# Kernel optimization log

Hardware: AMD Instinct MI355X
Metric: run time of the kernel (lower is better)

## Reference

```python
import jax, jax.numpy as jnp
import numpy as np

INPUT_DIM, HIDDEN_DIM, OUTPUT_DIM = 64, 256, 32
BATCH, SEQ = 256, 1024
# AutoNCP(256, 32, sparsity_level=0.5): motor=32, command=max(int(0.4*224),1)=89, inter=135
LAYER_HID = [135, 89, 32]
LAYER_IN = [INPUT_DIM, 135, 89]


def setup_inputs() -> dict:
    key = jax.random.key(0)
    ks = iter(jax.random.split(key, 64))
    d = {}
    d["x"] = jax.random.normal(next(ks), (BATCH, SEQ, INPUT_DIM), dtype=jnp.float32)
    for l, (fin, hid) in enumerate(zip(LAYER_IN, LAYER_HID)):
        sp = jax.random.bernoulli(next(ks), 0.5, (hid, fin))
        d[f"mask{l}"] = jnp.concatenate([sp, jnp.ones((hid, hid), dtype=bool)], axis=1)
        scale = 1.0 / np.sqrt(fin + hid)
        for name in ("W1", "W2", "Wa", "Wb"):
            d[f"{name}_{l}"] = jax.random.normal(next(ks), (hid, fin + hid), dtype=jnp.float32) * scale
        for name in ("b1", "b2", "ba", "bb"):
            d[f"{name}_{l}"] = jnp.zeros((hid,), dtype=jnp.float32)
    d["fc_W"] = jax.random.normal(next(ks), (HIDDEN_DIM, HIDDEN_DIM), dtype=jnp.float32) * (1.0 / np.sqrt(HIDDEN_DIM))
    d["fc_b"] = jnp.zeros((HIDDEN_DIM,), dtype=jnp.float32)
    return d


def _cfc_cell(inp, h, mask, W1, b1, W2, b2, Wa, ba, Wb, bb):
    # ncps CfCCell, mode='default', no backbone, ts = 1.0
    x = jnp.concatenate([inp, h], axis=1)
    m = mask.astype(W1.dtype)
    ff1 = jnp.tanh(x @ (W1 * m).T + b1)
    ff2 = jnp.tanh(x @ (W2 * m).T + b2)
    t = jax.nn.sigmoid(x @ Wa.T + ba + x @ Wb.T + bb)  # sigmoid(t_a*ts + t_b), ts=1
    return ff1 * (1.0 - t) + t * ff2


def _forward(x, masks, layer_params, fc_W, fc_b):
    B = x.shape[0]
    init = tuple(jnp.zeros((B, h), dtype=x.dtype) for h in LAYER_HID)

    def step(carry, xt):
        hs = list(carry)
        inp = xt
        for l in range(3):  # inter -> command -> motor (WiredCfCCell)
            hs[l] = _cfc_cell(inp, hs[l], masks[l], *layer_params[l])
            inp = hs[l]
        return tuple(hs), None

    carry, _ = jax.lax.scan(step, init, jnp.swapaxes(x, 0, 1))  # scan over time [T,B,D]
    hn = jnp.concatenate(carry, axis=1)  # [B, HIDDEN_DIM] full state
    return hn @ fc_W.T + fc_b


def reference(x, mask0, mask1, mask2,
              W1_0, b1_0, W2_0, b2_0, Wa_0, ba_0, Wb_0, bb_0,
              W1_1, b1_1, W2_1, b2_1, Wa_1, ba_1, Wb_1, bb_1,
              W1_2, b1_2, W2_2, b2_2, Wa_2, ba_2, Wb_2, bb_2,
              fc_W, fc_b):
    masks = (mask0, mask1, mask2)
    lp = ((W1_0, b1_0, W2_0, b2_0, Wa_0, ba_0, Wb_0, bb_0),
          (W1_1, b1_1, W2_1, b2_1, Wa_1, ba_1, Wb_1, bb_1),
          (W1_2, b1_2, W2_2, b2_2, Wa_2, ba_2, Wb_2, bb_2))
    return _forward(x, masks, lp, fc_W, fc_b)
```

## Files before the change

kernel.cpp:

```cpp
#include <hip/hip_runtime.h>


typedef _Float16 half2v __attribute__((ext_vector_type(2)));
typedef _Float16 half8v __attribute__((ext_vector_type(8)));
typedef int      int4v  __attribute__((ext_vector_type(4)));

#define NBLK   256
#define NTHR   512
#define TSTEPS 1024
#define KPAD   224
#define KHALF  112

struct Ptrs {
    const float* x;
    const unsigned int* msk[3];
    const float* W1[3];
    const float* W2[3];
    const float* Wa[3];
    const float* Wb[3];
    const float* b1[3];
    const float* b2[3];
    const float* ba[3];
    const float* bb[3];
    const float* fcW;
    const float* fcb;
};

__device__ __forceinline__ float fexp2(float x) {
#if __has_builtin(__builtin_amdgcn_exp2f)
    return __builtin_amdgcn_exp2f(x);
#else
    return exp2f(x);
#endif
}
__device__ __forceinline__ float frcp(float x) {
#if __has_builtin(__builtin_amdgcn_rcpf)
    return __builtin_amdgcn_rcpf(x);
#else
    return 1.0f / x;
#endif
}
__device__ __forceinline__ float fsig(float x) {
    return frcp(1.0f + fexp2(-1.442695041f * x));
}
__device__ __forceinline__ float ftanh(float x) {
    return 2.0f * frcp(1.0f + fexp2(-2.885390082f * x)) - 1.0f;
}

#if __has_builtin(__builtin_amdgcn_fdot2)
#define FD(a, b, c) __builtin_amdgcn_fdot2((a), (b), (c), false)
#else
__device__ __forceinline__ float fd_fallback(half2v a, half2v b, float c) {
    return c + (float)a[0] * (float)b[0] + (float)a[1] * (float)b[1];
}
#define FD(a, b, c) fd_fallback((a), (b), (c))
#endif

__device__ __forceinline__ half2v h2(_Float16 a, _Float16 b) { return half2v{a, b}; }

__device__ __forceinline__ half8v dpp_xor2(half8v v) {
    int4v a = __builtin_bit_cast(int4v, v);
    int4v r;
    r[0] = __builtin_amdgcn_update_dpp(0, a[0], 0x4E, 0xF, 0xF, true);
    r[1] = __builtin_amdgcn_update_dpp(0, a[1], 0x4E, 0xF, 0xF, true);
    r[2] = __builtin_amdgcn_update_dpp(0, a[2], 0x4E, 0xF, 0xF, true);
    r[3] = __builtin_amdgcn_update_dpp(0, a[3], 0x4E, 0xF, 0xF, true);
    return __builtin_bit_cast(half8v, r);
}
__device__ __forceinline__ float pair_sum(float x) {
    const int v = __builtin_amdgcn_update_dpp(
        0, __builtin_bit_cast(int, x), 0xB1, 0xF, 0xF, true);
    return x + __builtin_bit_cast(float, v);
}

__device__ __forceinline__ half2v fold2(const float* Wp, const unsigned int* mkp,
                                        int nK, int K, int k0) {
    float u0 = 0.f, u1 = 0.f;
    if (k0 < K) {
        const int i0 = nK + k0;
        u0 = Wp[i0] * ((mkp[i0] != 0u) ? 1.0f : 0.0f);
    }
    if (k0 + 1 < K) {
        const int i1 = nK + k0 + 1;
        u1 = Wp[i1] * ((mkp[i1] != 0u) ? 1.0f : 0.0f);
    }
    return h2((_Float16)u0, (_Float16)u1);
}

#define DOTS(m, xo_, xt_) { \
    const half2v o0 = h2(xo_[0], xo_[1]), o1 = h2(xo_[2], xo_[3]); \
    const half2v o2 = h2(xo_[4], xo_[5]), o3 = h2(xo_[6], xo_[7]); \
    const half2v t0 = h2(xt_[0], xt_[1]), t1 = h2(xt_[2], xt_[3]); \
    const half2v t2 = h2(xt_[4], xt_[5]), t3 = h2(xt_[6], xt_[7]); \
    ac00 = FD(o0, w1o[4*(m)+0], ac00);  ac01 = FD(t0, w1t[4*(m)+0], ac01); \
    ac10 = FD(o0, w2o[4*(m)+0], ac10);  ac11 = FD(t0, w2t[4*(m)+0], ac11); \
    ac20 = FD(o0, wao[4*(m)+0], ac20);  ac21 = FD(t0, wat[4*(m)+0], ac21); \
    ac00 = FD(o1, w1o[4*(m)+1], ac00);  ac01 = FD(t1, w1t[4*(m)+1], ac01); \
    ac10 = FD(o1, w2o[4*(m)+1], ac10);  ac11 = FD(t1, w2t[4*(m)+1], ac11); \
    ac20 = FD(o1, wao[4*(m)+1], ac20);  ac21 = FD(t1, wat[4*(m)+1], ac21); \
    ac00 = FD(o2, w1o[4*(m)+2], ac00);  ac01 = FD(t2, w1t[4*(m)+2], ac01); \
    ac10 = FD(o2, w2o[4*(m)+2], ac10);  ac11 = FD(t2, w2t[4*(m)+2], ac11); \
    ac20 = FD(o2, wao[4*(m)+2], ac20);  ac21 = FD(t2, wat[4*(m)+2], ac21); \
    ac00 = FD(o3, w1o[4*(m)+3], ac00);  ac01 = FD(t3, w1t[4*(m)+3], ac01); \
    ac10 = FD(o3, w2o[4*(m)+3], ac10);  ac11 = FD(t3, w2t[4*(m)+3], ac11); \
    ac20 = FD(o3, wao[4*(m)+3], ac20);  ac21 = FD(t3, wat[4*(m)+3], ac21); \
}

__global__ __launch_bounds__(NTHR)
__attribute__((amdgpu_waves_per_eu(2, 2)))
void cfc_kernel(Ptrs P, float* __restrict__ out) {
    __shared__ __align__(16) _Float16 xc[2][3][KPAD];
    __shared__ __align__(16) float hn[256];

    const int tid  = threadIdx.x;
    const int b    = blockIdx.x;
    const int unit = tid >> 1;
    const int half = tid & 1;
    const int up   = unit & 1;

    const bool direct = ((tid >> 6) == 4);

    int L, n;
    if (unit < 135)      { L = 0; n = unit; }
    else if (unit < 224) { L = 1; n = unit - 135; }
    else                 { L = 2; n = unit - 224; }
    const int K    = (L == 0) ? 199 : ((L == 1) ? 224 : 121);
    const int HOFF = (L == 0) ? 0   : ((L == 1) ? 135 : 224);

    {
        int* z = (int*)&xc[0][0][0];
        for (int i = tid; i < 2 * 3 * KPAD / 2; i += NTHR) z[i] = 0;
    }
    __syncthreads();

    const int xlane = tid - 448;
    float xpend = 0.0f;
    if (xlane >= 0) {
        xc[0][0][xlane] = (_Float16)P.x[((size_t)b * TSTEPS + 0) * 64 + xlane];
        xpend           = P.x[((size_t)b * TSTEPS + 1) * 64 + xlane];
    }

    const float* W1p        = P.W1[L];
    const float* W2p        = P.W2[L];
    const float* Wap        = P.Wa[L];
    const float* Wbp        = P.Wb[L];
    const unsigned int* mkp = P.msk[L];
    const int nK   = n * K;
    const int koff = half * KHALF;

    half2v w1o[28], w1t[28], w2o[28], w2t[28], wao[28], wat[28];
#pragma unroll
    for (int m = 0; m < 7; ++m) {
#pragma unroll
        for (int j = 0; j < 4; ++j) {
            const int ko = koff + (2 * m + up) * 8 + 2 * j;
            const int kt = koff + (2 * m + 1 - up) * 8 + 2 * j;
            w1o[m * 4 + j] = fold2(W1p, mkp, nK, K, ko);
            w1t[m * 4 + j] = fold2(W1p, mkp, nK, K, kt);
            w2o[m * 4 + j] = fold2(W2p, mkp, nK, K, ko);
            w2t[m * 4 + j] = fold2(W2p, mkp, nK, K, kt);
            {
                float a0 = 0.f, a1 = 0.f;
                if (ko < K)     a0 = Wap[nK + ko] + Wbp[nK + ko];
                if (ko + 1 < K) a1 = Wap[nK + ko + 1] + Wbp[nK + ko + 1];
                wao[m * 4 + j] = h2((_Float16)a0, (_Float16)a1);
            }
            {
                float a0 = 0.f, a1 = 0.f;
                if (kt < K)     a0 = Wap[nK + kt] + Wbp[nK + kt];
                if (kt + 1 < K) a1 = Wap[nK + kt + 1] + Wbp[nK + kt + 1];
                wat[m * 4 + j] = h2((_Float16)a0, (_Float16)a1);
            }
        }
    }
    const float bv1 = P.b1[L][n];
    const float bv2 = P.b2[L][n];
    const float bva = P.ba[L][n] + P.bb[L][n];
    __syncthreads();

    for (int tick = 0; tick < TSTEPS + 2; ++tick) {
        if (xlane >= 0) {
            if (tick + 1 < TSTEPS)
                xc[(tick + 1) & 1][0][xlane] = (_Float16)xpend;
            if (tick + 2 < TSTEPS)
                xpend = P.x[((size_t)b * TSTEPS + (tick + 2)) * 64 + xlane];
        }

        const int s = tick - L;
        if (s >= 0 && s < TSTEPS) {
            const _Float16* srcp = &xc[s & 1][L][koff];
            const _Float16* po   = srcp + up * 8;
            const _Float16* pt   = srcp + (1 - up) * 8;
            float ac00 = 0.f, ac01 = 0.f, ac10 = 0.f, ac11 = 0.f, ac20 = 0.f, ac21 = 0.f;
            if (!direct) {
#pragma unroll
                for (int m = 0; m < 7; ++m) {
                    const half8v xown = *(const half8v*)(po + m * 16);
                    const half8v xoth = dpp_xor2(xown);
                    DOTS(m, xown, xoth);
                }
            } else {
#pragma unroll
                for (int m = 0; m < 7; ++m) {
                    const half8v xown = *(const half8v*)(po + m * 16);
                    const half8v xoth = *(const half8v*)(pt + m * 16);
                    DOTS(m, xown, xoth);
                }
            }

            const float s1 = pair_sum(ac00 + ac01);
            const float s2 = pair_sum(ac10 + ac11);
            const float sa = pair_sum(ac20 + ac21);
            const float f1 = ftanh(s1 + bv1);
            const float f2 = ftanh(s2 + bv2);
            const float tg = fsig(sa + bva);
            const float h  = f1 + tg * (f2 - f1);
            const _Float16 hv = (_Float16)h;

            const int pA = s & 1;
            const int pB = (s + 1) & 1;
            if (half == 0) {
                if (L == 0)      xc[pA][1][n] = hv;
                else if (L == 1) xc[pA][2][n] = hv;
                if (s == TSTEPS - 1) hn[HOFF + n] = h;
            } else {
                if (L == 0)      xc[pB][0][64 + n]  = hv;
                else if (L == 1) xc[pB][1][135 + n] = hv;
                else             xc[pB][2][89 + n]  = hv;
            }
        }
        __syncthreads();
    }

    {
        const int o = unit;
        const float4* wr = (const float4*)(P.fcW + (size_t)o * 256 + half * 128);
        const float4* hr = (const float4*)(hn + half * 128);
        float acc = half ? 0.0f : P.fcb[o];
#pragma unroll 8
        for (int d = 0; d < 32; ++d) {
            const float4 a = hr[d];
            const float4 w = wr[d];
            acc += a.x * w.x + a.y * w.y + a.z * w.z + a.w * w.w;
        }
        acc = pair_sum(acc);
        if (half == 0) out[(size_t)b * 256 + o] = acc;
    }
}

extern "C" void kernel_launch(void* const* d_in, const int* in_sizes, int n_in,
                              void* d_out, int out_size, void* d_ws, size_t ws_size,
                              hipStream_t stream) {
    (void)in_sizes; (void)n_in; (void)out_size; (void)d_ws; (void)ws_size;
    Ptrs P;
    P.x = (const float*)d_in[0];
    for (int l = 0; l < 3; ++l) {
        const int base = 1 + l * 9;
        P.msk[l] = (const unsigned int*)d_in[base + 0];
        P.W1[l]  = (const float*)d_in[base + 1];
        P.W2[l]  = (const float*)d_in[base + 2];
        P.Wa[l]  = (const float*)d_in[base + 3];
        P.Wb[l]  = (const float*)d_in[base + 4];
        P.b1[l]  = (const float*)d_in[base + 5];
        P.b2[l]  = (const float*)d_in[base + 6];
        P.ba[l]  = (const float*)d_in[base + 7];
        P.bb[l]  = (const float*)d_in[base + 8];
    }
    P.fcW = (const float*)d_in[28];
    P.fcb = (const float*)d_in[29];

    hipLaunchKernelGGL(cfc_kernel, dim3(NBLK), dim3(NTHR), 0, stream,
                       P, (float*)d_out);
}
```

Baseline: 1.564 ms.

## Process two batch rows per block to reuse register-resident weights

Each block now handles two batch sequences instead of one, halving the grid to 128 blocks. The same register-held fp16 weights are applied to both rows' inputs each step, and the per-step barrier is shared between the two rows. The goal is to amortize the barrier and latency costs over twice the work. The trade-off is that only 128 blocks run on a GPU with more compute units, so part of the device sits idle, and per-step work doubles along the serial recurrence chain.

```diff
diff --git a/kernel.cpp b/kernel.cpp
--- a/kernel.cpp
+++ b/kernel.cpp
@@ -5,7 +5,7 @@
 typedef _Float16 half8v __attribute__((ext_vector_type(8)));
 typedef int      int4v  __attribute__((ext_vector_type(4)));
 
-#define NBLK   256
+#define NBLK   128
 #define NTHR   512
 #define TSTEPS 1024
 #define KPAD   224
@@ -87,30 +87,30 @@
     return h2((_Float16)u0, (_Float16)u1);
 }
 
-#define DOTS(m, xo_, xt_) { \
+#define DOTS(m, xo_, xt_, A0, A1, B0, B1, C0, C1) { \
     const half2v o0 = h2(xo_[0], xo_[1]), o1 = h2(xo_[2], xo_[3]); \
     const half2v o2 = h2(xo_[4], xo_[5]), o3 = h2(xo_[6], xo_[7]); \
     const half2v t0 = h2(xt_[0], xt_[1]), t1 = h2(xt_[2], xt_[3]); \
     const half2v t2 = h2(xt_[4], xt_[5]), t3 = h2(xt_[6], xt_[7]); \
-    ac00 = FD(o0, w1o[4*(m)+0], ac00);  ac01 = FD(t0, w1t[4*(m)+0], ac01); \
-    ac10 = FD(o0, w2o[4*(m)+0], ac10);  ac11 = FD(t0, w2t[4*(m)+0], ac11); \
-    ac20 = FD(o0, wao[4*(m)+0], ac20);  ac21 = FD(t0, wat[4*(m)+0], ac21); \
-    ac00 = FD(o1, w1o[4*(m)+1], ac00);  ac01 = FD(t1, w1t[4*(m)+1], ac01); \
-    ac10 = FD(o1, w2o[4*(m)+1], ac10);  ac11 = FD(t1, w2t[4*(m)+1], ac11); \
-    ac20 = FD(o1, wao[4*(m)+1], ac20);  ac21 = FD(t1, wat[4*(m)+1], ac21); \
-    ac00 = FD(o2, w1o[4*(m)+2], ac00);  ac01 = FD(t2, w1t[4*(m)+2], ac01); \
-    ac10 = FD(o2, w2o[4*(m)+2], ac10);  ac11 = FD(t2, w2t[4*(m)+2], ac11); \
-    ac20 = FD(o2, wao[4*(m)+2], ac20);  ac21 = FD(t2, wat[4*(m)+2], ac21); \
-    ac00 = FD(o3, w1o[4*(m)+3], ac00);  ac01 = FD(t3, w1t[4*(m)+3], ac01); \
-    ac10 = FD(o3, w2o[4*(m)+3], ac10);  ac11 = FD(t3, w2t[4*(m)+3], ac11); \
-    ac20 = FD(o3, wao[4*(m)+3], ac20);  ac21 = FD(t3, wat[4*(m)+3], ac21); \
+    A0 = FD(o0, w1o[4*(m)+0], A0);  A1 = FD(t0, w1t[4*(m)+0], A1); \
+    B0 = FD(o0, w2o[4*(m)+0], B0);  B1 = FD(t0, w2t[4*(m)+0], B1); \
+    C0 = FD(o0, wao[4*(m)+0], C0);  C1 = FD(t0, wat[4*(m)+0], C1); \
+    A0 = FD(o1, w1o[4*(m)+1], A0);  A1 = FD(t1, w1t[4*(m)+1], A1); \
+    B0 = FD(o1, w2o[4*(m)+1], B0);  B1 = FD(t1, w2t[4*(m)+1], B1); \
+    C0 = FD(o1, wao[4*(m)+1], C0);  C1 = FD(t1, wat[4*(m)+1], C1); \
+    A0 = FD(o2, w1o[4*(m)+2], A0);  A1 = FD(t2, w1t[4*(m)+2], A1); \
+    B0 = FD(o2, w2o[4*(m)+2], B0);  B1 = FD(t2, w2t[4*(m)+2], B1); \
+    C0 = FD(o2, wao[4*(m)+2], C0);  C1 = FD(t2, wat[4*(m)+2], C1); \
+    A0 = FD(o3, w1o[4*(m)+3], A0);  A1 = FD(t3, w1t[4*(m)+3], A1); \
+    B0 = FD(o3, w2o[4*(m)+3], B0);  B1 = FD(t3, w2t[4*(m)+3], B1); \
+    C0 = FD(o3, wao[4*(m)+3], C0);  C1 = FD(t3, wat[4*(m)+3], C1); \
 }
 
 __global__ __launch_bounds__(NTHR)
 __attribute__((amdgpu_waves_per_eu(2, 2)))
 void cfc_kernel(Ptrs P, float* __restrict__ out) {
-    __shared__ __align__(16) _Float16 xc[2][3][KPAD];
-    __shared__ __align__(16) float hn[256];
+    __shared__ __align__(16) _Float16 xc[2][2][3][KPAD];
+    __shared__ __align__(16) float hn[2][256];
 
     const int tid  = threadIdx.x;
     const int b    = blockIdx.x;
@@ -128,16 +128,19 @@
     const int HOFF = (L == 0) ? 0   : ((L == 1) ? 135 : 224);
 
     {
-        int* z = (int*)&xc[0][0][0];
-        for (int i = tid; i < 2 * 3 * KPAD / 2; i += NTHR) z[i] = 0;
+        int* z = (int*)&xc[0][0][0][0];
+        for (int i = tid; i < 2 * 2 * 3 * KPAD / 2; i += NTHR) z[i] = 0;
     }
     __syncthreads();
 
-    const int xlane = tid - 448;
+    const int xlane = tid - 384;
+    const int sr    = (xlane >> 6) & 1;
+    const int sf    = xlane & 63;
     float xpend = 0.0f;
     if (xlane >= 0) {
-        xc[0][0][xlane] = (_Float16)P.x[((size_t)b * TSTEPS + 0) * 64 + xlane];
-        xpend           = P.x[((size_t)b * TSTEPS + 1) * 64 + xlane];
+        const size_t rbase = ((size_t)(2 * b + sr)) * TSTEPS;
+        xc[sr][0][0][sf] = (_Float16)P.x[(rbase + 0) * 64 + sf];
+        xpend            = P.x[(rbase + 1) * 64 + sf];
     }
 
     const float* W1p        = P.W1[L];
@@ -181,61 +184,93 @@
     for (int tick = 0; tick < TSTEPS + 2; ++tick) {
         if (xlane >= 0) {
             if (tick + 1 < TSTEPS)
-                xc[(tick + 1) & 1][0][xlane] = (_Float16)xpend;
+                xc[sr][(tick + 1) & 1][0][sf] = (_Float16)xpend;
             if (tick + 2 < TSTEPS)
-                xpend = P.x[((size_t)b * TSTEPS + (tick + 2)) * 64 + xlane];
+                xpend = P.x[(((size_t)(2 * b + sr)) * TSTEPS + (tick + 2)) * 64 + sf];
         }
 
         const int s = tick - L;
         if (s >= 0 && s < TSTEPS) {
-            const _Float16* srcp = &xc[s & 1][L][koff];
-            const _Float16* po   = srcp + up * 8;
-            const _Float16* pt   = srcp + (1 - up) * 8;
-            float ac00 = 0.f, ac01 = 0.f, ac10 = 0.f, ac11 = 0.f, ac20 = 0.f, ac21 = 0.f;
+            const _Float16* s0 = &xc[0][s & 1][L][koff];
+            const _Float16* s1 = &xc[1][s & 1][L][koff];
+            const _Float16* po0 = s0 + up * 8;
+            const _Float16* pt0 = s0 + (1 - up) * 8;
+            const _Float16* po1 = s1 + up * 8;
+            const _Float16* pt1 = s1 + (1 - up) * 8;
+            float r000 = 0.f, r001 = 0.f, r010 = 0.f, r011 = 0.f, r020 = 0.f, r021 = 0.f;
+            float r100 = 0.f, r101 = 0.f, r110 = 0.f, r111 = 0.f, r120 = 0.f, r121 = 0.f;
             if (!direct) {
 #pragma unroll
                 for (int m = 0; m < 7; ++m) {
-                    const half8v xown = *(const half8v*)(po + m * 16);
-                    const half8v xoth = dpp_xor2(xown);
-                    DOTS(m, xown, xoth);
+                    const half8v x0o = *(const half8v*)(po0 + m * 16);
+                    const half8v x0t = dpp_xor2(x0o);
+                    const half8v x1o = *(const half8v*)(po1 + m * 16);
+                    const half8v x1t = dpp_xor2(x1o);
+                    DOTS(m, x0o, x0t, r000, r001, r010, r011, r020, r021);
+                    DOTS(m, x1o, x1t, r100, r101, r110, r111, r120, r121);
                 }
             } else {
 #pragma unroll
                 for (int m = 0; m < 7; ++m) {
-                    const half8v xown = *(const half8v*)(po + m * 16);
-                    const half8v xoth = *(const half8v*)(pt + m * 16);
-                    DOTS(m, xown, xoth);
+                    const half8v x0o = *(const half8v*)(po0 + m * 16);
+                    const half8v x0t = *(const half8v*)(pt0 + m * 16);
+                    const half8v x1o = *(const half8v*)(po1 + m * 16);
+                    const half8v x1t = *(const half8v*)(pt1 + m * 16);
+                    DOTS(m, x0o, x0t, r000, r001, r010, r011, r020, r021);
+                    DOTS(m, x1o, x1t, r100, r101, r110, r111, r120, r121);
                 }
             }
-
-            const float s1 = pair_sum(ac00 + ac01);
-            const float s2 = pair_sum(ac10 + ac11);
-            const float sa = pair_sum(ac20 + ac21);
-            const float f1 = ftanh(s1 + bv1);
-            const float f2 = ftanh(s2 + bv2);
-            const float tg = fsig(sa + bva);
-            const float h  = f1 + tg * (f2 - f1);
-            const _Float16 hv = (_Float16)h;
 
             const int pA = s & 1;
             const int pB = (s + 1) & 1;
-            if (half == 0) {
-                if (L == 0)      xc[pA][1][n] = hv;
-                else if (L == 1) xc[pA][2][n] = hv;
-                if (s == TSTEPS - 1) hn[HOFF + n] = h;
-            } else {
-                if (L == 0)      xc[pB][0][64 + n]  = hv;
-                else if (L == 1) xc[pB][1][135 + n] = hv;
-                else             xc[pB][2][89 + n]  = hv;
+
+            {
+                const float s1v = pair_sum(r000 + r001);
+                const float s2v = pair_sum(r010 + r011);
+                const float sav = pair_sum(r020 + r021);
+                const float f1 = ftanh(s1v + bv1);
+                const float f2 = ftanh(s2v + bv2);
+                const float tg = fsig(sav + bva);
+                const float h  = f1 + tg * (f2 - f1);
+                const _Float16 hv = (_Float16)h;
+                if (half == 0) {
+                    if (L == 0)      xc[0][pA][1][n] = hv;
+                    else if (L == 1) xc[0][pA][2][n] = hv;
+                    if (s == TSTEPS - 1) hn[0][HOFF + n] = h;
+                } else {
+                    if (L == 0)      xc[0][pB][0][64 + n]  = hv;
+                    else if (L == 1) xc[0][pB][1][135 + n] = hv;
+                    else             xc[0][pB][2][89 + n]  = hv;
+                }
+            }
+            {
+                const float s1v = pair_sum(r100 + r101);
+                const float s2v = pair_sum(r110 + r111);
+                const float sav = pair_sum(r120 + r121);
+                const float f1 = ftanh(s1v + bv1);
+                const float f2 = ftanh(s2v + bv2);
+                const float tg = fsig(sav + bva);
+                const float h  = f1 + tg * (f2 - f1);
+                const _Float16 hv = (_Float16)h;
+                if (half == 0) {
+                    if (L == 0)      xc[1][pA][1][n] = hv;
+                    else if (L == 1) xc[1][pA][2][n] = hv;
+                    if (s == TSTEPS - 1) hn[1][HOFF + n] = h;
+                } else {
+                    if (L == 0)      xc[1][pB][0][64 + n]  = hv;
+                    else if (L == 1) xc[1][pB][1][135 + n] = hv;
+                    else             xc[1][pB][2][89 + n]  = hv;
+                }
             }
         }
         __syncthreads();
     }
 
-    {
+#pragma unroll
+    for (int r = 0; r < 2; ++r) {
         const int o = unit;
         const float4* wr = (const float4*)(P.fcW + (size_t)o * 256 + half * 128);
-        const float4* hr = (const float4*)(hn + half * 128);
+        const float4* hr = (const float4*)(&hn[r][0] + half * 128);
         float acc = half ? 0.0f : P.fcb[o];
 #pragma unroll 8
         for (int d = 0; d < 32; ++d) {
@@ -244,7 +279,7 @@
             acc += a.x * w.x + a.y * w.y + a.z * w.z + a.w * w.w;
         }
         acc = pair_sum(acc);
-        if (half == 0) out[(size_t)b * 256 + o] = acc;
+        if (half == 0) out[((size_t)(2 * b + r)) * 256 + o] = acc;
     }
 }
 
```

New measurement: 2.382 ms. +52.3%, slower.
